# Performance work log

Measured on AMD Instinct MI355X. Metric: run time of the kernel, lower is better.

## Reference

```python
import jax, jax.numpy as jnp
import numpy as np

ALPHA = 1.0
INF = 1e4  # larger than any possible distance in a 256x256 image


def _row_dist_to_zero(x):
    """1D distance along last axis to nearest zero pixel. x: [..., W] (0/1)."""
    W = x.shape[-1]
    idx = jnp.arange(W, dtype=jnp.float32)
    is0 = x == 0
    # nearest zero at-or-before each position
    last0 = jax.lax.cummax(jnp.where(is0, idx, -1.0), axis=x.ndim - 1)
    fwd = jnp.where(last0 >= 0, idx - last0, INF)
    # nearest zero at-or-after each position (suffix max of -idx)
    neg_next0 = jax.lax.cummax(jnp.where(is0, -idx, -INF), axis=x.ndim - 1, reverse=True)
    bwd = jnp.where(neg_next0 > -INF, (-neg_next0) - idx, INF)
    return jnp.minimum(fwd, bwd)


def _edt_2d(target):
    """Exact Euclidean distance transform per [B,C] map: distance from nonzero
    pixels to nearest zero pixel (matches scipy.ndimage.distance_transform_edt)."""
    B, C, H, W = target.shape
    g = _row_dist_to_zero(target)            # [B,C,H,W] distance along width
    g2 = g * g
    i = jnp.arange(H, dtype=jnp.float32)
    dk2 = (i[:, None] - i[None, :]) ** 2     # [H(out), H(k)]
    # dt2[b,c,i,w] = min_k g2[b,c,k,w] + (i-k)^2
    d2 = jnp.min(g2[:, :, None, :, :] + dk2[None, None, :, :, None], axis=3)
    return jnp.sqrt(d2)


def _distance_map(target):
    dist = _edt_2d(target)
    dmax = jnp.max(dist, axis=(-2, -1), keepdims=True)
    return dist / (dmax + 1e-7)


def setup_inputs() -> dict:
    key = jax.random.key(0)
    k1, k2 = jax.random.split(key)
    pred = jax.random.normal(k1, (8, 1, 256, 256), dtype=jnp.float32)
    target = jax.random.randint(k2, (8, 1, 256, 256), 0, 2).astype(jnp.float32)
    return {"pred": pred, "target": target}


def reference(pred, target):
    dist_map = _distance_map(target)
    weight_map = 1.0 + ALPHA * dist_map
    # numerically stable BCE with logits, reduction='none'
    bce = jnp.maximum(pred, 0.0) - pred * target + jnp.log1p(jnp.exp(-jnp.abs(pred)))
    return jnp.mean(weight_map * bce)
```

## Files before the change

### kernel.cpp

```cpp
#include <hip/hip_runtime.h>
#include <math.h>

#define BATCH 8
#define H 256
#define W 256
#define NPIX (BATCH * H * W)
#define NBLK2 1024

__device__ float g_g2[NPIX];
__device__ float g_pmx[NBLK2];
__device__ float g_psb[NBLK2];
__device__ float g_psdb[NBLK2];

__device__ __forceinline__ float bce_logits(float p, float t) {
    return fmaxf(p, 0.0f) - p * t + log1pf(expf(-fabsf(p)));
}

__global__ void __launch_bounds__(256) row_edt(const float* __restrict__ target) {
    __shared__ unsigned long long mlds[4][4];
    const int tid = threadIdx.x;
    const int v = tid >> 6, l = tid & 63;
    const float* imgr = target + (size_t)blockIdx.x * 4 * W;

    #pragma unroll
    for (int j = 0; j < 4; ++j) {
        float t = imgr[j * W + tid];
        unsigned long long m = __ballot(t == 0.0f);
        if (l == 0) mlds[j][v] = m;
    }
    __syncthreads();

    const int p = tid;
    #pragma unroll
    for (int j = 0; j < 4; ++j) {
        unsigned long long mw[4] = {mlds[j][0], mlds[j][1], mlds[j][2], mlds[j][3]};
        int best = 1 << 20;
        #pragma unroll
        for (int w = 0; w < 4; ++w) {
            const int rel = p - (w << 6);
            const unsigned long long m = mw[w];
            unsigned long long mlo = (rel < 0)  ? 0ull
                                   : (rel >= 63) ? m : (m & ((2ull << rel) - 1ull));
            unsigned long long mhi = (rel <= 0) ? m
                                   : (rel > 63)  ? 0ull : (m & (~0ull << rel));
            if (mlo) best = min(best, rel - (63 - __builtin_clzll(mlo)));
            if (mhi) best = min(best, __builtin_ctzll(mhi) - rel);
        }
        float d = (best > 255) ? 1e4f : (float)best;
        g_g2[(size_t)blockIdx.x * 4 * W + j * W + tid] = d * d;
    }
}

__global__ void __launch_bounds__(256) envelope_bce(
        const float* __restrict__ pred, const float* __restrict__ target) {
    __shared__ float red[3][4];
    const int tid = threadIdx.x;
    const int wv = tid >> 6, l = tid & 63;
    const int b  = blockIdx.x >> 7;
    const int cs = (blockIdx.x >> 5) & 3;
    const int rs = blockIdx.x & 31;
    const int c  = (cs << 6) + l;
    const int i0 = (rs << 3) + (wv << 1);

    const size_t po = ((size_t)(b * H + i0)) * W + c;
    float p0 = pred[po], p1 = pred[po + W];
    float t0 = target[po], t1 = target[po + W];

    const float* gcol = g_g2 + (size_t)b * H * W + c;

    float acc0 = 3.0e38f, acc1 = 3.0e38f;
    const int P = 10;
    #pragma unroll
    for (int s = 0; s < P; ++s) {
        const int kd = i0 + 1 - s;
        const int ku = i0 + 2 + s;
        float gd = gcol[(size_t)max(kd, 0) * W];
        float gu = gcol[(size_t)min(ku, 255) * W];
        if (kd < 0)   gd = 3.0e38f;
        if (ku > 255) gu = 3.0e38f;
        const float ed0 = (float)(s - 1), ed1 = (float)s;
        const float eu0 = (float)(s + 2), eu1 = (float)(s + 1);
        acc0 = fminf(acc0, fminf(fmaf(ed0, ed0, gd), fmaf(eu0, eu0, gu)));
        acc1 = fminf(acc1, fminf(fmaf(ed1, ed1, gd), fmaf(eu1, eu1, gu)));
    }

    int kd = i0 + 1 - P, ku = i0 + 2 + P;
    float fd0 = (float)(i0 - kd);
    float fu0 = (float)(ku - i0);
    for (;;) {
        float maxacc = fmaxf(acc0, acc1);
        float dn = (float)(i0 - kd);
        float up = (float)(ku - (i0 + 1));
        bool alive = (kd >= 0 && dn * dn <= maxacc) || (ku <= 255 && up * up <= maxacc);
        if (!__any(alive)) break;
        if (kd >= 0) {
            float g = gcol[(size_t)kd * W];
            acc0 = fminf(acc0, fmaf(fd0, fd0, g));
            float fd1 = fd0 + 1.0f;
            acc1 = fminf(acc1, fmaf(fd1, fd1, g));
        }
        if (ku <= 255) {
            float g = gcol[(size_t)ku * W];
            float fu1 = fu0 - 1.0f;
            acc0 = fminf(acc0, fmaf(fu0, fu0, g));
            acc1 = fminf(acc1, fmaf(fu1, fu1, g));
        }
        --kd; ++ku; fd0 += 1.0f; fu0 += 1.0f;
    }

    float mx = fmaxf(acc0, acc1);
    float b0 = bce_logits(p0, t0), b1 = bce_logits(p1, t1);
    float sb  = b0 + b1;
    float sdb = sqrtf(acc0) * b0 + sqrtf(acc1) * b1;

    #pragma unroll
    for (int o = 32; o > 0; o >>= 1) {
        mx  = fmaxf(mx, __shfl_down(mx, o, 64));
        sb  += __shfl_down(sb, o, 64);
        sdb += __shfl_down(sdb, o, 64);
    }
    if (l == 0) { red[0][wv] = mx; red[1][wv] = sb; red[2][wv] = sdb; }
    __syncthreads();
    if (tid == 0) {
        g_pmx [blockIdx.x] = fmaxf(fmaxf(red[0][0], red[0][1]), fmaxf(red[0][2], red[0][3]));
        g_psb [blockIdx.x] = (red[1][0] + red[1][1]) + (red[1][2] + red[1][3]);
        g_psdb[blockIdx.x] = (red[2][0] + red[2][1]) + (red[2][2] + red[2][3]);
    }
}

__global__ void final_reduce(float* __restrict__ out) {
    const int tid = threadIdx.x;
    const int img = tid >> 5, j = tid & 31;
    float mx = 0.0f, sb = 0.0f, sdb = 0.0f;
    #pragma unroll
    for (int q = 0; q < 4; ++q) {
        const int e = (img << 7) + j + (q << 5);
        mx  = fmaxf(mx, g_pmx[e]);
        sb  += g_psb[e];
        sdb += g_psdb[e];
    }
    #pragma unroll
    for (int o = 16; o > 0; o >>= 1) {
        mx  = fmaxf(mx, __shfl_down(mx, o, 32));
        sb  += __shfl_down(sb, o, 32);
        sdb += __shfl_down(sdb, o, 32);
    }
    __shared__ float cimg[8], simg[8];
    if (j == 0) {
        cimg[img] = sdb / (sqrtf(mx) + 1e-7f);
        simg[img] = sb;
    }
    __syncthreads();
    if (tid == 0) {
        float tot = 0.0f;
        #pragma unroll
        for (int i = 0; i < 8; ++i) tot += simg[i] + cimg[i];
        out[0] = tot * (1.0f / (float)NPIX);
    }
}

extern "C" void kernel_launch(void* const* d_in, const int* in_sizes, int n_in,
                              void* d_out, int out_size, void* d_ws, size_t ws_size,
                              hipStream_t stream) {
    const float* pred   = (const float*)d_in[0];
    const float* target = (const float*)d_in[1];
    (void)d_ws; (void)ws_size;

    row_edt<<<BATCH * 64, 256, 0, stream>>>(target);
    envelope_bce<<<NBLK2, 256, 0, stream>>>(pred, target);
    final_reduce<<<1, 256, 0, stream>>>((float*)d_out);
}
```

Baseline: 66.28 us.

## Store row zero-bitmasks instead of g2 and recompute row distances on the fly

The first kernel now writes only 256-bit zero masks per row, not a full float g2 image. The envelope kernel stages a 32-row halo of masks in shared memory and recomputes each squared row distance from the bitmasks with clz/ctz on adjacent 64-bit words. Rows outside the halo fall back to loading masks from global memory. This removes the 2 MB g2 write and its strided column reads, at the cost of extra integer bit work per sample and a shared-memory sync.

```diff
diff --git a/kernel.cpp b/kernel.cpp
--- a/kernel.cpp
+++ b/kernel.cpp
@@ -6,8 +6,10 @@
 #define W 256
 #define NPIX (BATCH * H * W)
 #define NBLK2 1024
-
-__device__ float g_g2[NPIX];
+#define NROWS (BATCH * H)
+#define HALO 32
+
+__device__ unsigned long long g_masks[NROWS * 4];
 __device__ float g_pmx[NBLK2];
 __device__ float g_psb[NBLK2];
 __device__ float g_psdb[NBLK2];
@@ -16,29 +18,24 @@
     return fmaxf(p, 0.0f) - p * t + log1pf(expf(-fabsf(p)));
 }
 
-__global__ void __launch_bounds__(256) row_edt(const float* __restrict__ target) {
-    __shared__ unsigned long long mlds[4][4];
-    const int tid = threadIdx.x;
-    const int v = tid >> 6, l = tid & 63;
-    const float* imgr = target + (size_t)blockIdx.x * 4 * W;
-
-    #pragma unroll
-    for (int j = 0; j < 4; ++j) {
-        float t = imgr[j * W + tid];
-        unsigned long long m = __ballot(t == 0.0f);
-        if (l == 0) mlds[j][v] = m;
-    }
-    __syncthreads();
-
-    const int p = tid;
-    #pragma unroll
-    for (int j = 0; j < 4; ++j) {
-        unsigned long long mw[4] = {mlds[j][0], mlds[j][1], mlds[j][2], mlds[j][3]};
-        int best = 1 << 20;
+__device__ __forceinline__ float g2_win(const unsigned long long w[4], int cs, int l) {
+    const unsigned long long Wq = w[cs];
+    const unsigned long long Wm = (cs > 0) ? w[cs - 1] : 0ull;
+    const unsigned long long Wp = (cs < 3) ? w[cs + 1] : 0ull;
+    const unsigned long long down = (Wq << (63 - l)) | ((l == 63) ? 0ull : (Wm >> (l + 1)));
+    const unsigned long long up   = (Wq >> l) | ((l == 0) ? 0ull : (Wp << (64 - l)));
+    int best;
+    if (down | up) {
+        int dd = down ? __builtin_clzll(down) : (1 << 20);
+        int du = up   ? __builtin_ctzll(up)   : (1 << 20);
+        best = min(dd, du);
+    } else {
+        const int p = (cs << 6) + l;
+        best = 1 << 20;
         #pragma unroll
-        for (int w = 0; w < 4; ++w) {
-            const int rel = p - (w << 6);
-            const unsigned long long m = mw[w];
+        for (int q = 0; q < 4; ++q) {
+            const int rel = p - (q << 6);
+            const unsigned long long m = w[q];
             unsigned long long mlo = (rel < 0)  ? 0ull
                                    : (rel >= 63) ? m : (m & ((2ull << rel) - 1ull));
             unsigned long long mhi = (rel <= 0) ? m
@@ -46,13 +43,29 @@
             if (mlo) best = min(best, rel - (63 - __builtin_clzll(mlo)));
             if (mhi) best = min(best, __builtin_ctzll(mhi) - rel);
         }
-        float d = (best > 255) ? 1e4f : (float)best;
-        g_g2[(size_t)blockIdx.x * 4 * W + j * W + tid] = d * d;
+    }
+    float d = (best > 255) ? 1e4f : (float)best;
+    return d * d;
+}
+
+__global__ void __launch_bounds__(256) make_masks(const float* __restrict__ target) {
+    const int wv = threadIdx.x >> 6, l = threadIdx.x & 63;
+    const int r = blockIdx.x * 4 + wv;
+    const float* trow = target + (size_t)r * W;
+    float t0 = trow[l], t1 = trow[l + 64], t2 = trow[l + 128], t3 = trow[l + 192];
+    unsigned long long m0 = __ballot(t0 == 0.0f);
+    unsigned long long m1 = __ballot(t1 == 0.0f);
+    unsigned long long m2 = __ballot(t2 == 0.0f);
+    unsigned long long m3 = __ballot(t3 == 0.0f);
+    if (l < 4) {
+        unsigned long long m = (l == 0) ? m0 : (l == 1) ? m1 : (l == 2) ? m2 : m3;
+        g_masks[(size_t)r * 4 + l] = m;
     }
 }
 
 __global__ void __launch_bounds__(256) envelope_bce(
         const float* __restrict__ pred, const float* __restrict__ target) {
+    __shared__ unsigned long long mh[HALO][4];
     __shared__ float red[3][4];
     const int tid = threadIdx.x;
     const int wv = tid >> 6, l = tid & 63;
@@ -61,12 +74,19 @@
     const int rs = blockIdx.x & 31;
     const int c  = (cs << 6) + l;
     const int i0 = (rs << 3) + (wv << 1);
+    const int hlo = (rs << 3) - 12;
 
     const size_t po = ((size_t)(b * H + i0)) * W + c;
     float p0 = pred[po], p1 = pred[po + W];
     float t0 = target[po], t1 = target[po + W];
 
-    const float* gcol = g_g2 + (size_t)b * H * W + c;
+    if (tid < HALO * 4) {
+        const int hr = hlo + (tid >> 2);
+        unsigned long long m = 0ull;
+        if (hr >= 0 && hr < H) m = g_masks[(((size_t)(b * H + hr)) << 2) | (tid & 3)];
+        mh[tid >> 2][tid & 3] = m;
+    }
+    __syncthreads();
 
     float acc0 = 3.0e38f, acc1 = 3.0e38f;
     const int P = 10;
@@ -74,10 +94,8 @@
     for (int s = 0; s < P; ++s) {
         const int kd = i0 + 1 - s;
         const int ku = i0 + 2 + s;
-        float gd = gcol[(size_t)max(kd, 0) * W];
-        float gu = gcol[(size_t)min(ku, 255) * W];
-        if (kd < 0)   gd = 3.0e38f;
-        if (ku > 255) gu = 3.0e38f;
+        float gd = g2_win(mh[kd - hlo], cs, l);
+        float gu = g2_win(mh[ku - hlo], cs, l);
         const float ed0 = (float)(s - 1), ed1 = (float)s;
         const float eu0 = (float)(s + 2), eu1 = (float)(s + 1);
         acc0 = fminf(acc0, fminf(fmaf(ed0, ed0, gd), fmaf(eu0, eu0, gu)));
@@ -94,13 +112,27 @@
         bool alive = (kd >= 0 && dn * dn <= maxacc) || (ku <= 255 && up * up <= maxacc);
         if (!__any(alive)) break;
         if (kd >= 0) {
-            float g = gcol[(size_t)kd * W];
+            float g;
+            if (kd >= hlo) g = g2_win(mh[kd - hlo], cs, l);
+            else {
+                unsigned long long w[4];
+                #pragma unroll
+                for (int q = 0; q < 4; ++q) w[q] = g_masks[(((size_t)(b * H + kd)) << 2) | q];
+                g = g2_win(w, cs, l);
+            }
             acc0 = fminf(acc0, fmaf(fd0, fd0, g));
             float fd1 = fd0 + 1.0f;
             acc1 = fminf(acc1, fmaf(fd1, fd1, g));
         }
         if (ku <= 255) {
-            float g = gcol[(size_t)ku * W];
+            float g;
+            if (ku - hlo < HALO) g = g2_win(mh[ku - hlo], cs, l);
+            else {
+                unsigned long long w[4];
+                #pragma unroll
+                for (int q = 0; q < 4; ++q) w[q] = g_masks[(((size_t)(b * H + ku)) << 2) | q];
+                g = g2_win(w, cs, l);
+            }
             float fu1 = fu0 - 1.0f;
             acc0 = fminf(acc0, fmaf(fu0, fu0, g));
             acc1 = fminf(acc1, fmaf(fu1, fu1, g));
@@ -166,7 +198,7 @@
     const float* target = (const float*)d_in[1];
     (void)d_ws; (void)ws_size;
 
-    row_edt<<<BATCH * 64, 256, 0, stream>>>(target);
+    make_masks<<<NROWS / 4, 256, 0, stream>>>(target);
     envelope_bce<<<NBLK2, 256, 0, stream>>>(pred, target);
     final_reduce<<<1, 256, 0, stream>>>((float*)d_out);
 }
```

After: 72.03 us. +8.7%, slower.
